# Kernel optimization log

Hardware: AMD Instinct MI355X
Metric: run time of the kernel (lower is better)

The kernel has to match this reference:

```python
import jax, jax.numpy as jnp
import numpy as np

NC, M, D = 4, 512, 64
COMMITMENT_COST = 0.25


def setup_inputs() -> dict:
    key = jax.random.key(0)
    k1, k2 = jax.random.split(key)
    N = 65536
    x = jax.random.normal(k1, (N, NC * D), dtype=jnp.float32)
    # original init: uniform(-1/m, 1/m); randn*small keeps comparable scale
    embedding = jax.random.normal(k2, (NC, M, D), dtype=jnp.float32) * (1.0 / M)
    mask = jnp.ones((N, NC), dtype=jnp.float32)
    return {"x": x, "embedding": embedding, "mask": mask}


def reference(x, embedding, mask):
    nc, m, d = embedding.shape
    x_flat = x.reshape(-1, nc, d)                      # (N, nc, d)
    xd = jax.lax.stop_gradient(x_flat)                 # detached copy

    # squared-distance search expressed as a GEMM (same math as sum((x-e)^2)):
    x2 = jnp.sum(xd * xd, axis=-1)[:, :, None]
    e2 = jnp.sum(embedding * embedding, axis=-1)[None, :, :]
    xe = jnp.einsum('ncd,cmd->ncm', xd, embedding)
    distances = x2 - 2.0 * xe + e2

    indices = jnp.argmin(distances, axis=-1)           # (N, nc) int
    # gather nearest code vectors: (N, nc, d)
    quantized = embedding[jnp.arange(nc)[None, :], indices]
    quantized = quantized * mask[..., None]

    codebook_loss = jnp.mean((jax.lax.stop_gradient(x_flat) - quantized) ** 2)
    e_latent_loss = jnp.mean((x_flat - jax.lax.stop_gradient(quantized)) ** 2)
    commitment_loss = COMMITMENT_COST * e_latent_loss

    # straight-through estimator
    quantized_st = x_flat + jax.lax.stop_gradient(quantized - x_flat)
    quantized_st = quantized_st.reshape(x.shape)

    # perplexity via per-codebook histogram (avoids N x nc x m one-hot)
    counts = jax.vmap(lambda idx: jnp.bincount(idx, length=m))(indices.T)  # (nc, m)
    avg_probs = counts.astype(x.dtype) / x_flat.shape[0]
    perplexity = jnp.exp(-jnp.sum(avg_probs * jnp.log(avg_probs + 1e-10)))

    return (quantized_st, commitment_loss, codebook_loss, perplexity, indices)
```

## Files before the change

### kernel.cpp

```cpp
#include <hip/hip_runtime.h>
#include <math.h>
#include <float.h>

#define NTOK 65536
#define NCB  4
#define MCODE 512
#define DIM  64

#define QST_SIZE (NTOK * NCB * DIM)
#define IDX_OFF  (QST_SIZE + 3)

#define TOK_TILE  128

#define WS_EH 0
#define WS_EL 262144
#define WS_D0 524288
#define WS_CNT 532480
#define WS_LOSS 540672

typedef _Float16 half8 __attribute__((ext_vector_type(8)));
typedef float floatx16 __attribute__((ext_vector_type(16)));

__global__ __launch_bounds__(256) void prep_kernel(const float* __restrict__ emb,
                                                   _Float16* __restrict__ ehf,
                                                   _Float16* __restrict__ elf,
                                                   float* __restrict__ d0p,
                                                   int* __restrict__ counts,
                                                   float* __restrict__ lossSum) {
    const int tid  = threadIdx.x;
    const int lane = tid & 63;
    const int row  = blockIdx.x * 4 + (tid >> 6);
    const int c    = row >> 9;
    const int n    = row & 511;
    const int nt   = n >> 5;
    const int r5   = n & 31;

    const float e = emb[(size_t)row * DIM + lane];

    float s = e * e;
#pragma unroll
    for (int off = 32; off > 0; off >>= 1) s += __shfl_xor(s, off);

    const float f = e * 512.0f;
    const _Float16 hv = (_Float16)f;
    const _Float16 lv = (_Float16)(f - (float)hv);

    const int ch = lane >> 4;
    const int h  = (lane >> 3) & 1;
    const int t  = lane & 7;
    const size_t off = ((size_t)((c * 16 + nt) * 4 + ch)) * 512 + (h * 32 + r5) * 8 + t;
    ehf[off] = hv;
    elf[off] = lv;

    if (lane == 0) {
        d0p[row] = -256.0f * s;
        counts[row] = 0;
        if (row == 0) *lossSum = 0.f;
    }
}

__global__ __launch_bounds__(256) void vq_main(const float* __restrict__ x,
                                               const float* __restrict__ emb,
                                               const float* __restrict__ mask,
                                               const _Float16* __restrict__ ehf,
                                               const _Float16* __restrict__ elf,
                                               const float* __restrict__ d0p,
                                               int* __restrict__ counts,
                                               float* __restrict__ lossSum,
                                               float* __restrict__ outQ,
                                               float* __restrict__ outIdx) {
    __shared__ __align__(16) _Float16 As[2][4096];
    __shared__ __align__(16) float d0s[MCODE];
    __shared__ int   Is[TOK_TILE];
    __shared__ float wls[4];

    const int tid  = threadIdx.x;
    const int c    = blockIdx.y;
    const int n0tk = blockIdx.x * TOK_TILE;
    const int lane = tid & 63;
    const int w    = tid >> 6;
    const int l31  = lane & 31;
    const int hi   = lane >> 5;
    const int hi4  = hi * 4;

    const _Float16* gEh = ehf + (size_t)c * (16 * 4 * 512);
    const _Float16* gEl = elf + (size_t)c * (16 * 4 * 512);

    float4 sh = *(const float4*)(gEh + tid * 8);
    float4 sl = *(const float4*)(gEl + tid * 8);
    float4 dstage;
    if (tid < 128) dstage = *(const float4*)(d0p + c * MCODE + tid * 4);

    half8 Bh[4], Bl[4];
    {
        const float* xr = x + (size_t)(n0tk + w * 32 + l31) * (NCB * DIM) + c * DIM + hi * 8;
#pragma unroll
        for (int ch = 0; ch < 4; ++ch) {
            float fv[8];
            *(float4*)(fv)     = *(const float4*)(xr + ch * 16);
            *(float4*)(fv + 4) = *(const float4*)(xr + ch * 16 + 4);
            half8 h8, l8;
#pragma unroll
            for (int t = 0; t < 8; ++t) {
                float f = fv[t];
                _Float16 hh = (_Float16)f;
                h8[t] = hh;
                l8[t] = (_Float16)(f - (float)hh);
            }
            Bh[ch] = h8;
            Bl[ch] = l8;
        }
    }

    *(float4*)((char*)&As[0][0]    + tid * 16) = sh;
    *(float4*)((char*)&As[0][2048] + tid * 16) = sl;
    if (tid < 128) *(float4*)(&d0s[tid * 4]) = dstage;
    __syncthreads();

    float maxv = -FLT_MAX;
    int   maxn = 0;

    for (int nt = 0; nt < 16; ++nt) {
        const int p = nt & 1;

        float4 nh, nl;
        if (nt < 15) {
            nh = *(const float4*)(gEh + (nt + 1) * 2048 + tid * 8);
            nl = *(const float4*)(gEl + (nt + 1) * 2048 + tid * 8);
        }

        const _Float16* ah = &As[p][0] + lane * 8;
        const _Float16* al = &As[p][2048] + lane * 8;
        half8 Ah0 = *(const half8*)(ah);
        half8 Ah1 = *(const half8*)(ah + 512);
        half8 Ah2 = *(const half8*)(ah + 1024);
        half8 Ah3 = *(const half8*)(ah + 1536);
        half8 Al0 = *(const half8*)(al);
        half8 Al1 = *(const half8*)(al + 512);
        half8 Al2 = *(const half8*)(al + 1024);
        half8 Al3 = *(const half8*)(al + 1536);

        const float* dpt = &d0s[nt * 32 + hi4];
        float4 d40 = *(const float4*)(dpt);
        float4 d41 = *(const float4*)(dpt + 8);
        float4 d42 = *(const float4*)(dpt + 16);
        float4 d43 = *(const float4*)(dpt + 24);
        floatx16 acc;
        acc[0]  = d40.x; acc[1]  = d40.y; acc[2]  = d40.z; acc[3]  = d40.w;
        acc[4]  = d41.x; acc[5]  = d41.y; acc[6]  = d41.z; acc[7]  = d41.w;
        acc[8]  = d42.x; acc[9]  = d42.y; acc[10] = d42.z; acc[11] = d42.w;
        acc[12] = d43.x; acc[13] = d43.y; acc[14] = d43.z; acc[15] = d43.w;

        acc = __builtin_amdgcn_mfma_f32_32x32x16_f16(Ah0, Bh[0], acc, 0, 0, 0);
        acc = __builtin_amdgcn_mfma_f32_32x32x16_f16(Al0, Bh[0], acc, 0, 0, 0);
        acc = __builtin_amdgcn_mfma_f32_32x32x16_f16(Ah0, Bl[0], acc, 0, 0, 0);
        acc = __builtin_amdgcn_mfma_f32_32x32x16_f16(Ah1, Bh[1], acc, 0, 0, 0);
        acc = __builtin_amdgcn_mfma_f32_32x32x16_f16(Al1, Bh[1], acc, 0, 0, 0);
        acc = __builtin_amdgcn_mfma_f32_32x32x16_f16(Ah1, Bl[1], acc, 0, 0, 0);
        acc = __builtin_amdgcn_mfma_f32_32x32x16_f16(Ah2, Bh[2], acc, 0, 0, 0);
        acc = __builtin_amdgcn_mfma_f32_32x32x16_f16(Al2, Bh[2], acc, 0, 0, 0);
        acc = __builtin_amdgcn_mfma_f32_32x32x16_f16(Ah2, Bl[2], acc, 0, 0, 0);
        acc = __builtin_amdgcn_mfma_f32_32x32x16_f16(Ah3, Bh[3], acc, 0, 0, 0);
        acc = __builtin_amdgcn_mfma_f32_32x32x16_f16(Al3, Bh[3], acc, 0, 0, 0);
        acc = __builtin_amdgcn_mfma_f32_32x32x16_f16(Ah3, Bl[3], acc, 0, 0, 0);

        const int nbase = nt * 32 + hi4;
#pragma unroll
        for (int r = 0; r < 16; ++r) {
            float m = acc[r];
            int   n = nbase + ((r & 3) + 8 * (r >> 2));
            if (m > maxv) { maxv = m; maxn = n; }
        }

        if (nt < 15) {
            *(float4*)((char*)&As[p ^ 1][0]    + tid * 16) = nh;
            *(float4*)((char*)&As[p ^ 1][2048] + tid * 16) = nl;
        }
        __syncthreads();
    }

    {
        float ov = __shfl_xor(maxv, 32);
        int   on = __shfl_xor(maxn, 32);
        if (ov > maxv || (ov == maxv && on < maxn)) { maxv = ov; maxn = on; }
    }

    if (hi == 0) {
        Is[w * 32 + l31] = maxn;
        atomicAdd(&counts[c * MCODE + maxn], 1);
        outIdx[(size_t)(n0tk + w * 32 + l31) * NCB + c] = (float)maxn;
    }
    __syncthreads();

    float lloss = 0.f;
#pragma unroll
    for (int i = 0; i < 8; ++i) {
        int q = tid + i * 256;
        int tok = q >> 4, d4 = q & 15;
        int idx = Is[tok];
        float mv = mask[(size_t)(n0tk + tok) * NCB + c];
        float4 e4 = *(const float4*)(emb + ((size_t)c * MCODE + idx) * DIM + d4 * 4);
        float4 x4 = *(const float4*)(x + (size_t)(n0tk + tok) * (NCB * DIM) + c * DIM + d4 * 4);
        float qx = e4.x * mv, qy = e4.y * mv, qz = e4.z * mv, qw = e4.w * mv;
        float4 o;
        o.x = x4.x + (qx - x4.x);
        o.y = x4.y + (qy - x4.y);
        o.z = x4.z + (qz - x4.z);
        o.w = x4.w + (qw - x4.w);
        *(float4*)(outQ + (size_t)(n0tk + tok) * (NCB * DIM) + c * DIM + d4 * 4) = o;
        float dx = x4.x - qx, dy = x4.y - qy, dz = x4.z - qz, dw = x4.w - qw;
        lloss += dx * dx + dy * dy + dz * dz + dw * dw;
    }
#pragma unroll
    for (int off = 32; off > 0; off >>= 1) lloss += __shfl_xor(lloss, off);
    if ((tid & 63) == 0) wls[tid >> 6] = lloss;
    __syncthreads();
    if (tid == 0) {
        float s = wls[0] + wls[1] + wls[2] + wls[3];
        atomicAdd(lossSum, s);
    }
}

__global__ __launch_bounds__(256) void finalize_kernel(const int* __restrict__ counts,
                                                       const float* __restrict__ lossSum,
                                                       float* __restrict__ out) {
    __shared__ float wls[4];
    int tid = threadIdx.x;
    float s = 0.f;
#pragma unroll
    for (int i = 0; i < 8; ++i) {
        int j = tid + i * 256;
        float p = (float)counts[j] * (1.0f / 65536.0f);
        s += p * logf(p + 1e-10f);
    }
#pragma unroll
    for (int off = 32; off > 0; off >>= 1) s += __shfl_xor(s, off);
    if ((tid & 63) == 0) wls[tid >> 6] = s;
    __syncthreads();
    if (tid == 0) {
        float tot = wls[0] + wls[1] + wls[2] + wls[3];
        float L = *lossSum * (1.0f / (float)QST_SIZE);
        out[QST_SIZE + 0] = 0.25f * L;
        out[QST_SIZE + 1] = L;
        out[QST_SIZE + 2] = expf(-tot);
    }
}

extern "C" void kernel_launch(void* const* d_in, const int* in_sizes, int n_in,
                              void* d_out, int out_size, void* d_ws, size_t ws_size,
                              hipStream_t stream) {
    const float* x    = (const float*)d_in[0];
    const float* emb  = (const float*)d_in[1];
    const float* mask = (const float*)d_in[2];
    float* out = (float*)d_out;

    _Float16* ehf  = (_Float16*)((char*)d_ws + WS_EH);
    _Float16* elf  = (_Float16*)((char*)d_ws + WS_EL);
    float* d0p     = (float*)((char*)d_ws + WS_D0);
    int*   counts  = (int*)((char*)d_ws + WS_CNT);
    float* lossSum = (float*)((char*)d_ws + WS_LOSS);

    prep_kernel<<<dim3(512), dim3(256), 0, stream>>>(emb, ehf, elf, d0p, counts, lossSum);
    vq_main<<<dim3(NTOK / TOK_TILE, NCB), dim3(256), 0, stream>>>(
        x, emb, mask, ehf, elf, d0p, counts, lossSum, out, out + IDX_OFF);
    finalize_kernel<<<dim3(1), dim3(256), 0, stream>>>(counts, lossSum, out);
}
```

Measured before the change: 198.5 us.

## Process two token sub-tiles per wave to reuse codebook fragments

```diff
diff --git a/kernel.cpp b/kernel.cpp
--- a/kernel.cpp
+++ b/kernel.cpp
@@ -10,7 +10,7 @@
 #define QST_SIZE (NTOK * NCB * DIM)
 #define IDX_OFF  (QST_SIZE + 3)
 
-#define TOK_TILE  128
+#define TOK_TILE  256
 
 #define WS_EH 0
 #define WS_EL 262144
@@ -91,9 +91,10 @@
     float4 dstage;
     if (tid < 128) dstage = *(const float4*)(d0p + c * MCODE + tid * 4);
 
-    half8 Bh[4], Bl[4];
-    {
-        const float* xr = x + (size_t)(n0tk + w * 32 + l31) * (NCB * DIM) + c * DIM + hi * 8;
+    half8 B0h[4], B0l[4], B1h[4], B1l[4];
+#pragma unroll
+    for (int s = 0; s < 2; ++s) {
+        const float* xr = x + (size_t)(n0tk + w * 64 + s * 32 + l31) * (NCB * DIM) + c * DIM + hi * 8;
 #pragma unroll
         for (int ch = 0; ch < 4; ++ch) {
             float fv[8];
@@ -107,8 +108,8 @@
                 h8[t] = hh;
                 l8[t] = (_Float16)(f - (float)hh);
             }
-            Bh[ch] = h8;
-            Bl[ch] = l8;
+            if (s == 0) { B0h[ch] = h8; B0l[ch] = l8; }
+            else        { B1h[ch] = h8; B1l[ch] = l8; }
         }
     }
 
@@ -117,8 +118,8 @@
     if (tid < 128) *(float4*)(&d0s[tid * 4]) = dstage;
     __syncthreads();
 
-    float maxv = -FLT_MAX;
-    int   maxn = 0;
+    float maxv0 = -FLT_MAX, maxv1 = -FLT_MAX;
+    int   maxn0 = 0,        maxn1 = 0;
 
     for (int nt = 0; nt < 16; ++nt) {
         const int p = nt & 1;
@@ -145,31 +146,46 @@
         float4 d41 = *(const float4*)(dpt + 8);
         float4 d42 = *(const float4*)(dpt + 16);
         float4 d43 = *(const float4*)(dpt + 24);
-        floatx16 acc;
-        acc[0]  = d40.x; acc[1]  = d40.y; acc[2]  = d40.z; acc[3]  = d40.w;
-        acc[4]  = d41.x; acc[5]  = d41.y; acc[6]  = d41.z; acc[7]  = d41.w;
-        acc[8]  = d42.x; acc[9]  = d42.y; acc[10] = d42.z; acc[11] = d42.w;
-        acc[12] = d43.x; acc[13] = d43.y; acc[14] = d43.z; acc[15] = d43.w;
-
-        acc = __builtin_amdgcn_mfma_f32_32x32x16_f16(Ah0, Bh[0], acc, 0, 0, 0);
-        acc = __builtin_amdgcn_mfma_f32_32x32x16_f16(Al0, Bh[0], acc, 0, 0, 0);
-        acc = __builtin_amdgcn_mfma_f32_32x32x16_f16(Ah0, Bl[0], acc, 0, 0, 0);
-        acc = __builtin_amdgcn_mfma_f32_32x32x16_f16(Ah1, Bh[1], acc, 0, 0, 0);
-        acc = __builtin_amdgcn_mfma_f32_32x32x16_f16(Al1, Bh[1], acc, 0, 0, 0);
-        acc = __builtin_amdgcn_mfma_f32_32x32x16_f16(Ah1, Bl[1], acc, 0, 0, 0);
-        acc = __builtin_amdgcn_mfma_f32_32x32x16_f16(Ah2, Bh[2], acc, 0, 0, 0);
-        acc = __builtin_amdgcn_mfma_f32_32x32x16_f16(Al2, Bh[2], acc, 0, 0, 0);
-        acc = __builtin_amdgcn_mfma_f32_32x32x16_f16(Ah2, Bl[2], acc, 0, 0, 0);
-        acc = __builtin_amdgcn_mfma_f32_32x32x16_f16(Ah3, Bh[3], acc, 0, 0, 0);
-        acc = __builtin_amdgcn_mfma_f32_32x32x16_f16(Al3, Bh[3], acc, 0, 0, 0);
-        acc = __builtin_amdgcn_mfma_f32_32x32x16_f16(Ah3, Bl[3], acc, 0, 0, 0);
+        floatx16 acc0, acc1;
+        acc0[0]  = d40.x; acc0[1]  = d40.y; acc0[2]  = d40.z; acc0[3]  = d40.w;
+        acc0[4]  = d41.x; acc0[5]  = d41.y; acc0[6]  = d41.z; acc0[7]  = d41.w;
+        acc0[8]  = d42.x; acc0[9]  = d42.y; acc0[10] = d42.z; acc0[11] = d42.w;
+        acc0[12] = d43.x; acc0[13] = d43.y; acc0[14] = d43.z; acc0[15] = d43.w;
+        acc1 = acc0;
+
+        acc0 = __builtin_amdgcn_mfma_f32_32x32x16_f16(Ah0, B0h[0], acc0, 0, 0, 0);
+        acc1 = __builtin_amdgcn_mfma_f32_32x32x16_f16(Ah0, B1h[0], acc1, 0, 0, 0);
+        acc0 = __builtin_amdgcn_mfma_f32_32x32x16_f16(Al0, B0h[0], acc0, 0, 0, 0);
+        acc1 = __builtin_amdgcn_mfma_f32_32x32x16_f16(Al0, B1h[0], acc1, 0, 0, 0);
+        acc0 = __builtin_amdgcn_mfma_f32_32x32x16_f16(Ah0, B0l[0], acc0, 0, 0, 0);
+        acc1 = __builtin_amdgcn_mfma_f32_32x32x16_f16(Ah0, B1l[0], acc1, 0, 0, 0);
+        acc0 = __builtin_amdgcn_mfma_f32_32x32x16_f16(Ah1, B0h[1], acc0, 0, 0, 0);
+        acc1 = __builtin_amdgcn_mfma_f32_32x32x16_f16(Ah1, B1h[1], acc1, 0, 0, 0);
+        acc0 = __builtin_amdgcn_mfma_f32_32x32x16_f16(Al1, B0h[1], acc0, 0, 0, 0);
+        acc1 = __builtin_amdgcn_mfma_f32_32x32x16_f16(Al1, B1h[1], acc1, 0, 0, 0);
+        acc0 = __builtin_amdgcn_mfma_f32_32x32x16_f16(Ah1, B0l[1], acc0, 0, 0, 0);
+        acc1 = __builtin_amdgcn_mfma_f32_32x32x16_f16(Ah1, B1l[1], acc1, 0, 0, 0);
+        acc0 = __builtin_amdgcn_mfma_f32_32x32x16_f16(Ah2, B0h[2], acc0, 0, 0, 0);
+        acc1 = __builtin_amdgcn_mfma_f32_32x32x16_f16(Ah2, B1h[2], acc1, 0, 0, 0);
+        acc0 = __builtin_amdgcn_mfma_f32_32x32x16_f16(Al2, B0h[2], acc0, 0, 0, 0);
+        acc1 = __builtin_amdgcn_mfma_f32_32x32x16_f16(Al2, B1h[2], acc1, 0, 0, 0);
+        acc0 = __builtin_amdgcn_mfma_f32_32x32x16_f16(Ah2, B0l[2], acc0, 0, 0, 0);
+        acc1 = __builtin_amdgcn_mfma_f32_32x32x16_f16(Ah2, B1l[2], acc1, 0, 0, 0);
+        acc0 = __builtin_amdgcn_mfma_f32_32x32x16_f16(Ah3, B0h[3], acc0, 0, 0, 0);
+        acc1 = __builtin_amdgcn_mfma_f32_32x32x16_f16(Ah3, B1h[3], acc1, 0, 0, 0);
+        acc0 = __builtin_amdgcn_mfma_f32_32x32x16_f16(Al3, B0h[3], acc0, 0, 0, 0);
+        acc1 = __builtin_amdgcn_mfma_f32_32x32x16_f16(Al3, B1h[3], acc1, 0, 0, 0);
+        acc0 = __builtin_amdgcn_mfma_f32_32x32x16_f16(Ah3, B0l[3], acc0, 0, 0, 0);
+        acc1 = __builtin_amdgcn_mfma_f32_32x32x16_f16(Ah3, B1l[3], acc1, 0, 0, 0);
 
         const int nbase = nt * 32 + hi4;
 #pragma unroll
         for (int r = 0; r < 16; ++r) {
-            float m = acc[r];
-            int   n = nbase + ((r & 3) + 8 * (r >> 2));
-            if (m > maxv) { maxv = m; maxn = n; }
+            const int n = nbase + ((r & 3) + 8 * (r >> 2));
+            float m0 = acc0[r];
+            float m1 = acc1[r];
+            if (m0 > maxv0) { maxv0 = m0; maxn0 = n; }
+            if (m1 > maxv1) { maxv1 = m1; maxn1 = n; }
         }
 
         if (nt < 15) {
@@ -180,21 +196,27 @@
     }
 
     {
-        float ov = __shfl_xor(maxv, 32);
-        int   on = __shfl_xor(maxn, 32);
-        if (ov > maxv || (ov == maxv && on < maxn)) { maxv = ov; maxn = on; }
+        float ov = __shfl_xor(maxv0, 32);
+        int   on = __shfl_xor(maxn0, 32);
+        if (ov > maxv0 || (ov == maxv0 && on < maxn0)) { maxv0 = ov; maxn0 = on; }
+        ov = __shfl_xor(maxv1, 32);
+        on = __shfl_xor(maxn1, 32);
+        if (ov > maxv1 || (ov == maxv1 && on < maxn1)) { maxv1 = ov; maxn1 = on; }
     }
 
     if (hi == 0) {
-        Is[w * 32 + l31] = maxn;
-        atomicAdd(&counts[c * MCODE + maxn], 1);
-        outIdx[(size_t)(n0tk + w * 32 + l31) * NCB + c] = (float)maxn;
+        Is[w * 64 + l31]      = maxn0;
+        Is[w * 64 + 32 + l31] = maxn1;
+        atomicAdd(&counts[c * MCODE + maxn0], 1);
+        atomicAdd(&counts[c * MCODE + maxn1], 1);
+        outIdx[(size_t)(n0tk + w * 64 + l31) * NCB + c]      = (float)maxn0;
+        outIdx[(size_t)(n0tk + w * 64 + 32 + l31) * NCB + c] = (float)maxn1;
     }
     __syncthreads();
 
     float lloss = 0.f;
 #pragma unroll
-    for (int i = 0; i < 8; ++i) {
+    for (int i = 0; i < 16; ++i) {
         int q = tid + i * 256;
         int tok = q >> 4, d4 = q & 15;
         int idx = Is[tok];
```

After: 218.8 us. +10.3%, slower.
